# Optimization experiments

Measured on AMD Instinct MI355X. Metric: run time of the kernel, lower is better.

## Reference

```python
import jax, jax.numpy as jnp
import numpy as np

T, H, E, F, K, FS = 2048, 2048, 64, 512, 8, 512


def setup_inputs() -> dict:
    key = jax.random.key(0)
    ks = jax.random.split(key, 6)
    s = 0.02
    return {
        "hidden_states": jax.random.normal(ks[0], (T, H), jnp.float32),
        # merged gate: E router logits + 1 shared-expert gate logit
        "W_gate": jax.random.normal(ks[1], (H, E + 1), jnp.float32) * s,
        # per-expert merged gate_up proj: [E, H, 2F]
        "W_gate_up": jax.random.normal(ks[2], (E, H, 2 * F), jnp.float32) * s,
        "W_down": jax.random.normal(ks[3], (E, F, H), jnp.float32) * s,
        # shared expert
        "Ws_gate_up": jax.random.normal(ks[4], (H, 2 * FS), jnp.float32) * s,
        "Ws_down": jax.random.normal(ks[5], (FS, H), jnp.float32) * s,
    }


def reference(hidden_states, W_gate, W_gate_up, W_down, Ws_gate_up, Ws_down):
    x = hidden_states  # [T, H]
    logits_all = x @ W_gate                      # [T, E+1]
    router_logits = logits_all[:, :E]
    shared_gate_logit = logits_all[:, E:]        # [T, 1]

    # FusedMoE routing: softmax -> top_k -> renormalize (norm_topk_prob=True)
    probs = jax.nn.softmax(router_logits.astype(jnp.float32), axis=-1)
    topk_w, topk_idx = jax.lax.top_k(probs, K)   # [T, K]
    topk_w = topk_w / jnp.sum(topk_w, axis=-1, keepdims=True)
    # dense combine weights [T, E] (zero for unselected experts)
    combine = jnp.zeros((T, E), probs.dtype).at[
        jnp.arange(T)[:, None], topk_idx].set(topk_w)

    # grouped expert GEMMs (dense reference: every expert sees all tokens,
    # combine-weights zero-out unrouted pairs)
    gu = jnp.einsum('th,ehf->etf', x, W_gate_up)   # [E, T, 2F]
    g, u = jnp.split(gu, 2, axis=-1)
    act = jax.nn.silu(g) * u                       # [E, T, F]
    # apply combine weight before down-proj to avoid [E, T, H] intermediate
    act = act * combine.T[:, :, None].astype(act.dtype)
    routed = jnp.einsum('etf,efh->th', act, W_down)  # [T, H]

    # shared expert (Qwen3NextMLP with sigmoid expert_gate)
    sgu = x @ Ws_gate_up                           # [T, 2FS]
    sg, su = jnp.split(sgu, 2, axis=-1)
    shared = (jax.nn.silu(sg) * su) @ Ws_down      # [T, H]
    shared = jax.nn.sigmoid(shared_gate_logit) * shared

    return shared + routed.astype(x.dtype)
```

## Files before the change

kernel.cpp:

```cpp
#include <hip/hip_runtime.h>
#include <hip/hip_bf16.h>
#include <math.h>

#define T_TOK 2048
#define H_DIM 2048
#define E_NUM 64
#define F_DIM 512
#define K_TOP 8
#define FS_DIM 512
#define NROWS (T_TOK * K_TOP)

typedef __attribute__((ext_vector_type(8))) short short8v;
typedef __attribute__((ext_vector_type(4))) float f32x4;

static __device__ __forceinline__ unsigned short f2bf(float f) {
    unsigned int u = __float_as_uint(f);
    u += 0x7fff + ((u >> 16) & 1);
    return (unsigned short)(u >> 16);
}

#define BCHUNK(row, k8) ((((k8) ^ ((row) + ((row) >> 3)))) & 7)
#define ASW32(r) (((r) >> 1) & 3)

typedef const unsigned int __attribute__((address_space(1))) gu32;
typedef unsigned int __attribute__((address_space(3))) lu32;
#define GLDS16(gsrc, ldst) \
    __builtin_amdgcn_global_load_lds((gu32*)(gsrc), (lu32*)(ldst), 16, 0, 0)

__global__ __launch_bounds__(256) void cvt_bf16_kernel(
    const float* __restrict__ in, unsigned short* __restrict__ out, int n8)
{
    int i = blockIdx.x * 256 + threadIdx.x;
    if (i < n8) {
        const float4* p = (const float4*)(in + (size_t)i * 8);
        float4 v0 = p[0], v1 = p[1];
        ushort4 a = make_ushort4(f2bf(v0.x), f2bf(v0.y), f2bf(v0.z), f2bf(v0.w));
        ushort4 b = make_ushort4(f2bf(v1.x), f2bf(v1.y), f2bf(v1.z), f2bf(v1.w));
        ushort4* q = (ushort4*)(out + (size_t)i * 8);
        q[0] = a; q[1] = b;
    }
}

__global__ __launch_bounds__(64) void router_kernel(
    const float* __restrict__ x, const float* __restrict__ Wg,
    int* __restrict__ topk_idx, float* __restrict__ topk_w,
    float* __restrict__ sgate, int* __restrict__ counts)
{
    const int t = blockIdx.x;
    const int lane = threadIdx.x;
    const float* xr = x + (size_t)t * H_DIM;

    float a0 = 0.f, a1 = 0.f, a2 = 0.f, a3 = 0.f;
    for (int h = 0; h < H_DIM; h += 4) {
        float4 xv = *(const float4*)&xr[h];
        a0 += xv.x * Wg[(h + 0) * 65 + lane];
        a1 += xv.y * Wg[(h + 1) * 65 + lane];
        a2 += xv.z * Wg[(h + 2) * 65 + lane];
        a3 += xv.w * Wg[(h + 3) * 65 + lane];
    }
    float logit = (a0 + a1) + (a2 + a3);

    float a64 = 0.f;
    for (int h = lane; h < H_DIM; h += 64) a64 += xr[h] * Wg[h * 65 + 64];
#pragma unroll
    for (int off = 32; off >= 1; off >>= 1) a64 += __shfl_xor(a64, off);

    float v = logit;
    float selv[K_TOP]; int seli[K_TOP];
#pragma unroll
    for (int k = 0; k < K_TOP; ++k) {
        float mv = v; int mi = lane;
#pragma unroll
        for (int off = 32; off >= 1; off >>= 1) {
            float ov = __shfl_xor(mv, off);
            int   oi = __shfl_xor(mi, off);
            if (ov > mv || (ov == mv && oi < mi)) { mv = ov; mi = oi; }
        }
        selv[k] = mv; seli[k] = mi;
        if (lane == mi) v = -INFINITY;
    }

    if (lane == 0) {
        float m = selv[0];
        float w[K_TOP]; float s = 0.f;
#pragma unroll
        for (int k = 0; k < K_TOP; ++k) { w[k] = __expf(selv[k] - m); s += w[k]; }
        float inv = 1.f / s;
#pragma unroll
        for (int k = 0; k < K_TOP; ++k) {
            topk_idx[t * K_TOP + k] = seli[k];
            topk_w[t * K_TOP + k] = w[k] * inv;
            atomicAdd(&counts[seli[k]], 1);
        }
        sgate[t] = 1.f / (1.f + __expf(-a64));
    }
}

__global__ __launch_bounds__(256) void bucket_kernel(
    const int* __restrict__ topk_idx, const float* __restrict__ topk_w,
    const int* __restrict__ counts, int* __restrict__ offsets,
    int* __restrict__ bucket_tok, float* __restrict__ bucket_w)
{
    const int e = blockIdx.x, thr = threadIdx.x;
    __shared__ int cnt[256];
    __shared__ int base_s;
    const int q0 = thr * 64;
    int c = 0;
    for (int q = 0; q < 64; ++q) c += (topk_idx[q0 + q] == e) ? 1 : 0;
    cnt[thr] = c;
    __syncthreads();
    if (thr == 0) {
        int off = 0;
        for (int i = 0; i < e; ++i) off += counts[i];
        offsets[e] = off;
        base_s = off;
        int run = 0;
        for (int i = 0; i < 256; ++i) { int tval = cnt[i]; cnt[i] = run; run += tval; }
    }
    __syncthreads();
    int pos = base_s + cnt[thr];
    for (int q = 0; q < 64; ++q) {
        int pp = q0 + q;
        if (topk_idx[pp] == e) {
            bucket_tok[pos] = pp >> 3;
            bucket_w[pos] = topk_w[pp];
            ++pos;
        }
    }
}

template<bool ROUTED>
__global__ __launch_bounds__(512, 4) void gu_mfma_kernel(
    const unsigned short* __restrict__ xb,
    const float* __restrict__ Wall,
    const int* __restrict__ counts, const int* __restrict__ offsets,
    const int* __restrict__ bucket_tok, const float* __restrict__ bucket_w,
    unsigned short* __restrict__ actout)
{
    constexpr int BM = 256;
    __shared__ __align__(16) unsigned short As[2][BM * 32];
    __shared__ __align__(16) unsigned short Bs[2][128 * 64];
    __shared__ int   toksS[BM];
    __shared__ float twsS[BM];

    const int tid  = threadIdx.x;
    const int lane = tid & 63;
    const int wid  = tid >> 6;
    const int wm = wid >> 1, wn = wid & 1;
    const int lrow = lane & 15, lhi = lane >> 4;

    int cblk, mt, ne, base;
    const float* W;
    if (ROUTED) {
        int nw = (blockIdx.x & 7) * ((int)gridDim.x >> 3) + (blockIdx.x >> 3);
        int e = nw >> 4; mt = (nw >> 3) & 1; cblk = nw & 7;
        ne = counts[e]; base = offsets[e];
        if (mt * BM >= ne) return;
        W = Wall + (size_t)e * H_DIM * (2 * F_DIM);
    } else {
        cblk = blockIdx.x; mt = blockIdx.y;
        ne = T_TOK; base = 0;
        W = Wall;
    }
    const int c0 = cblk * 64;

    const int n4 = (tid & 31) * 4;
    const int kq = (tid >> 5) * 4;
    const int grp = n4 >> 5;
    const int srccol = c0 + (grp >> 1) * 32 + (n4 & 31) + ((grp & 1) ? F_DIM : 0);
    int wrB[4];
#pragma unroll
    for (int cc = 0; cc < 4; ++cc) {
        int n = n4 + cc;
        wrB[cc] = n * 64 + BCHUNK(n, kq >> 3) * 8 + (kq & 7);
    }
    int rdB[4][2];
#pragma unroll
    for (int fn = 0; fn < 4; ++fn) {
        int r = wn * 64 + fn * 16 + lrow;
#pragma unroll
        for (int ks = 0; ks < 2; ++ks) {
            int kc = ks * 4 + lhi;
            rdB[fn][ks] = r * 64 + BCHUNK(r, kc) * 8;
        }
    }
    int rdA[4];
#pragma unroll
    for (int fm = 0; fm < 4; ++fm) {
        int arow = wm * 64 + fm * 16 + lrow;
        rdA[fm] = arow * 32 + ((lhi ^ ASW32(arow)) << 3);
    }
    const int ar0 = wid * 32 + (lane >> 2);
    const int ar1 = ar0 + 16;
    const int NT   = H_DIM / 64;
    const int SMAX = H_DIM / 32;
    const int m0_stride = ROUTED ? (2 * BM) : ((int)gridDim.y * BM);

    for (int m0 = mt * BM; m0 < ne; m0 += m0_stride) {
        __syncthreads();
        if (tid < BM) {
            int idx = m0 + tid; bool v = idx < ne;
            if (ROUTED) {
                toksS[tid] = v ? bucket_tok[base + idx] : bucket_tok[base];
                twsS[tid]  = v ? bucket_w[base + idx] : 0.f;
            } else {
                toksS[tid] = v ? idx : (T_TOK - 1);
                twsS[tid]  = 1.f;
            }
        }
        __syncthreads();

        const int src0 = toksS[ar0] * H_DIM + (((lane & 3) ^ ASW32(ar0)) << 3);
        const int src1 = toksS[ar1] * H_DIM + (((lane & 3) ^ ASW32(ar1)) << 3);

        f32x4 acc[4][4];
#pragma unroll
        for (int i = 0; i < 4; ++i)
#pragma unroll
            for (int j = 0; j < 4; ++j) acc[i][j] = (f32x4){0.f, 0.f, 0.f, 0.f};

        float4 bq[4];
#pragma unroll
        for (int i = 0; i < 4; ++i)
            bq[i] = *(const float4*)&W[(size_t)(kq + i) * (2 * F_DIM) + srccol];
        GLDS16(xb + src0, &As[0][(wid * 32) * 32]);
        GLDS16(xb + src1, &As[0][(wid * 32 + 16) * 32]);
#pragma unroll
        for (int cc = 0; cc < 4; ++cc)
            *(ushort4*)&Bs[0][wrB[cc]] = make_ushort4(
                f2bf(((const float*)&bq[0])[cc]), f2bf(((const float*)&bq[1])[cc]),
                f2bf(((const float*)&bq[2])[cc]), f2bf(((const float*)&bq[3])[cc]));
#pragma unroll
        for (int i = 0; i < 4; ++i)
            bq[i] = *(const float4*)&W[(size_t)(64 + kq + i) * (2 * F_DIM) + srccol];
        __syncthreads();

        for (int s = 0; s < SMAX; ++s) {
            const int kt = s >> 1;
            if (s + 1 < SMAX) {
                const int kof = (s + 1) * 32;
                GLDS16(xb + src0 + kof, &As[(s + 1) & 1][(wid * 32) * 32]);
                GLDS16(xb + src1 + kof, &As[(s + 1) & 1][(wid * 32 + 16) * 32]);
            }
            if ((s & 1) && (kt + 1 < NT)) {
#pragma unroll
                for (int cc = 0; cc < 4; ++cc)
                    *(ushort4*)&Bs[(kt + 1) & 1][wrB[cc]] = make_ushort4(
                        f2bf(((const float*)&bq[0])[cc]), f2bf(((const float*)&bq[1])[cc]),
                        f2bf(((const float*)&bq[2])[cc]), f2bf(((const float*)&bq[3])[cc]));
                int knx = (kt + 2 < NT) ? (kt + 2) * 64 : (NT - 1) * 64;
#pragma unroll
                for (int i = 0; i < 4; ++i)
                    bq[i] = *(const float4*)&W[(size_t)(knx + kq + i) * (2 * F_DIM) + srccol];
            }
            __builtin_amdgcn_sched_barrier(0);
            const unsigned short* A_ = As[s & 1];
            const unsigned short* B_ = Bs[kt & 1];
            const int ks = s & 1;
            short8v bf[4];
#pragma unroll
            for (int fn = 0; fn < 4; ++fn) bf[fn] = *(const short8v*)&B_[rdB[fn][ks]];
#pragma unroll
            for (int fm = 0; fm < 4; ++fm) {
                short8v af = *(const short8v*)&A_[rdA[fm]];
#pragma unroll
                for (int fn = 0; fn < 4; ++fn)
                    acc[fm][fn] = __builtin_amdgcn_mfma_f32_16x16x32_bf16(af, bf[fn], acc[fm][fn], 0, 0, 0);
            }
            __syncthreads();
        }

#pragma unroll
        for (int fm = 0; fm < 4; ++fm) {
#pragma unroll
            for (int p = 0; p < 2; ++p) {
                const int acol = c0 + wn * 32 + p * 16 + lrow;
#pragma unroll
                for (int i = 0; i < 4; ++i) {
                    int ml = wm * 64 + fm * 16 + lhi * 4 + i;
                    int idx = m0 + ml;
                    if (idx < ne) {
                        float gv = acc[fm][p][i], uv = acc[fm][p + 2][i];
                        float sg = gv / (1.f + __expf(-gv));
                        float val = sg * uv * twsS[ml];
                        size_t orow = ROUTED ? (size_t)(base + idx) : (size_t)idx;
                        actout[orow * F_DIM + acol] = f2bf(val);
                    }
                }
            }
        }
    }
}

template<bool ROUTED>
__global__ __launch_bounds__(512, 4) void down_mfma_kernel(
    const unsigned short* __restrict__ actb,
    const float* __restrict__ Wall,
    const int* __restrict__ counts, const int* __restrict__ offsets,
    const int* __restrict__ bucket_tok, const float* __restrict__ sgate,
    float* __restrict__ out)
{
    constexpr int BM = 256;
    __shared__ __align__(16) unsigned short As[2][BM * 32];
    __shared__ __align__(16) unsigned short Bs[2][128 * 64];
    __shared__ int   toksS[BM];
    __shared__ float sgS[BM];

    const int tid  = threadIdx.x;
    const int lane = tid & 63;
    const int wid  = tid >> 6;
    const int wm = wid >> 1, wn = wid & 1;
    const int lrow = lane & 15, lhi = lane >> 4;

    int cblk, mt, ne, base;
    const float* W;
    if (ROUTED) {
        int nw = (blockIdx.x & 7) * ((int)gridDim.x >> 3) + (blockIdx.x >> 3);
        int e = nw >> 5; mt = (nw >> 4) & 1; cblk = nw & 15;
        ne = counts[e]; base = offsets[e];
        if (mt * BM >= ne) return;
        W = Wall + (size_t)e * F_DIM * H_DIM;
    } else {
        cblk = blockIdx.x; mt = blockIdx.y;
        ne = T_TOK; base = 0;
        W = Wall;
    }
    const int c0 = cblk * 128;

    const int n4 = (tid & 31) * 4;
    const int kq = (tid >> 5) * 4;
    const int srccol = c0 + n4;
    int wrB[4];
#pragma unroll
    for (int cc = 0; cc < 4; ++cc) {
        int n = n4 + cc;
        wrB[cc] = n * 64 + BCHUNK(n, kq >> 3) * 8 + (kq & 7);
    }
    int rdB[4][2];
#pragma unroll
    for (int fn = 0; fn < 4; ++fn) {
        int r = wn * 64 + fn * 16 + lrow;
#pragma unroll
        for (int ks = 0; ks < 2; ++ks) {
            int kc = ks * 4 + lhi;
            rdB[fn][ks] = r * 64 + BCHUNK(r, kc) * 8;
        }
    }
    int rdA[4];
#pragma unroll
    for (int fm = 0; fm < 4; ++fm) {
        int arow = wm * 64 + fm * 16 + lrow;
        rdA[fm] = arow * 32 + ((lhi ^ ASW32(arow)) << 3);
    }
    const int ar0 = wid * 32 + (lane >> 2);
    const int ar1 = ar0 + 16;
    const int NT   = F_DIM / 64;
    const int SMAX = F_DIM / 32;
    const int m0_stride = ROUTED ? (2 * BM) : ((int)gridDim.y * BM);

    for (int m0 = mt * BM; m0 < ne; m0 += m0_stride) {
        __syncthreads();
        if (tid < BM) {
            int idx = m0 + tid;
            if (ROUTED) {
                toksS[tid] = (idx < ne) ? bucket_tok[base + idx] : 0;
            } else {
                sgS[tid] = sgate[(idx < ne) ? idx : (T_TOK - 1)];
            }
        }
        __syncthreads();

        int g0 = ROUTED ? min(base + m0 + ar0, NROWS - 1) : min(m0 + ar0, T_TOK - 1);
        int g1 = ROUTED ? min(base + m0 + ar1, NROWS - 1) : min(m0 + ar1, T_TOK - 1);
        const int src0 = g0 * F_DIM + (((lane & 3) ^ ASW32(ar0)) << 3);
        const int src1 = g1 * F_DIM + (((lane & 3) ^ ASW32(ar1)) << 3);

        f32x4 acc[4][4];
#pragma unroll
        for (int i = 0; i < 4; ++i)
#pragma unroll
            for (int j = 0; j < 4; ++j) acc[i][j] = (f32x4){0.f, 0.f, 0.f, 0.f};

        float4 bq[4];
#pragma unroll
        for (int i = 0; i < 4; ++i)
            bq[i] = *(const float4*)&W[(size_t)(kq + i) * H_DIM + srccol];
        GLDS16(actb + src0, &As[0][(wid * 32) * 32]);
        GLDS16(actb + src1, &As[0][(wid * 32 + 16) * 32]);
#pragma unroll
        for (int cc = 0; cc < 4; ++cc)
            *(ushort4*)&Bs[0][wrB[cc]] = make_ushort4(
                f2bf(((const float*)&bq[0])[cc]), f2bf(((const float*)&bq[1])[cc]),
                f2bf(((const float*)&bq[2])[cc]), f2bf(((const float*)&bq[3])[cc]));
#pragma unroll
        for (int i = 0; i < 4; ++i)
            bq[i] = *(const float4*)&W[(size_t)(64 + kq + i) * H_DIM + srccol];
        __syncthreads();

        for (int s = 0; s < SMAX; ++s) {
            const int kt = s >> 1;
            if (s + 1 < SMAX) {
                const int kof = (s + 1) * 32;
                GLDS16(actb + src0 + kof, &As[(s + 1) & 1][(wid * 32) * 32]);
                GLDS16(actb + src1 + kof, &As[(s + 1) & 1][(wid * 32 + 16) * 32]);
            }
            if ((s & 1) && (kt + 1 < NT)) {
#pragma unroll
                for (int cc = 0; cc < 4; ++cc)
                    *(ushort4*)&Bs[(kt + 1) & 1][wrB[cc]] = make_ushort4(
                        f2bf(((const float*)&bq[0])[cc]), f2bf(((const float*)&bq[1])[cc]),
                        f2bf(((const float*)&bq[2])[cc]), f2bf(((const float*)&bq[3])[cc]));
                int knx = (kt + 2 < NT) ? (kt + 2) * 64 : (NT - 1) * 64;
#pragma unroll
                for (int i = 0; i < 4; ++i)
                    bq[i] = *(const float4*)&W[(size_t)(knx + kq + i) * H_DIM + srccol];
            }
            __builtin_amdgcn_sched_barrier(0);
            const unsigned short* A_ = As[s & 1];
            const unsigned short* B_ = Bs[kt & 1];
            const int ks = s & 1;
            short8v bf[4];
#pragma unroll
            for (int fn = 0; fn < 4; ++fn) bf[fn] = *(const short8v*)&B_[rdB[fn][ks]];
#pragma unroll
            for (int fm = 0; fm < 4; ++fm) {
                short8v af = *(const short8v*)&A_[rdA[fm]];
#pragma unroll
                for (int fn = 0; fn < 4; ++fn)
                    acc[fm][fn] = __builtin_amdgcn_mfma_f32_16x16x32_bf16(af, bf[fn], acc[fm][fn], 0, 0, 0);
            }
            __syncthreads();
        }

#pragma unroll
        for (int fm = 0; fm < 4; ++fm) {
#pragma unroll
            for (int fn = 0; fn < 4; ++fn) {
                int col = c0 + wn * 64 + fn * 16 + lrow;
#pragma unroll
                for (int i = 0; i < 4; ++i) {
                    int ml = wm * 64 + fm * 16 + lhi * 4 + i;
                    int idx = m0 + ml;
                    if (idx < ne) {
                        if (ROUTED) {
                            atomicAdd(&out[(size_t)toksS[ml] * H_DIM + col], acc[fm][fn][i]);
                        } else {
                            out[(size_t)idx * H_DIM + col] = sgS[ml] * acc[fm][fn][i];
                        }
                    }
                }
            }
        }
    }
}

extern "C" void kernel_launch(void* const* d_in, const int* in_sizes, int n_in,
                              void* d_out, int out_size, void* d_ws, size_t ws_size,
                              hipStream_t stream) {
    const float* x    = (const float*)d_in[0];
    const float* Wg   = (const float*)d_in[1];
    const float* Wgu  = (const float*)d_in[2];
    const float* Wd   = (const float*)d_in[3];
    const float* Wsgu = (const float*)d_in[4];
    const float* Wsd  = (const float*)d_in[5];
    float* out = (float*)d_out;

    char* p = (char*)d_ws;
    auto alloc = [&](size_t bytes) {
        char* r = p;
        p += (bytes + 255) & ~(size_t)255;
        return r;
    };
    int*   topk_idx   = (int*)  alloc((size_t)T_TOK * K_TOP * sizeof(int));
    float* topk_w     = (float*)alloc((size_t)T_TOK * K_TOP * sizeof(float));
    float* sgate      = (float*)alloc((size_t)T_TOK * sizeof(float));
    int*   counts     = (int*)  alloc((size_t)E_NUM * sizeof(int));
    int*   offsets    = (int*)  alloc((size_t)E_NUM * sizeof(int));
    int*   bucket_tok = (int*)  alloc((size_t)NROWS * sizeof(int));
    float* bucket_w   = (float*)alloc((size_t)NROWS * sizeof(float));
    unsigned short* xb    = (unsigned short*)alloc((size_t)T_TOK * H_DIM * sizeof(short));
    unsigned short* act_r = (unsigned short*)alloc((size_t)NROWS * F_DIM * sizeof(short));
    unsigned short* act_s = (unsigned short*)alloc((size_t)T_TOK * FS_DIM * sizeof(short));

    hipMemsetAsync(counts, 0, E_NUM * sizeof(int), stream);
    cvt_bf16_kernel<<<(T_TOK * H_DIM / 8 + 255) / 256, 256, 0, stream>>>(x, xb, T_TOK * H_DIM / 8);
    router_kernel<<<T_TOK, 64, 0, stream>>>(x, Wg, topk_idx, topk_w, sgate, counts);
    bucket_kernel<<<E_NUM, 256, 0, stream>>>(topk_idx, topk_w, counts, offsets, bucket_tok, bucket_w);

    gu_mfma_kernel<true><<<8 * E_NUM * 2, 512, 0, stream>>>(
        xb, Wgu, counts, offsets, bucket_tok, bucket_w, act_r);
    gu_mfma_kernel<false><<<dim3(8, T_TOK / 256), 512, 0, stream>>>(
        xb, Wsgu, counts, offsets, bucket_tok, bucket_w, act_s);

    down_mfma_kernel<false><<<dim3(16, T_TOK / 256), 512, 0, stream>>>(
        act_s, Wsd, counts, offsets, bucket_tok, sgate, out);
    down_mfma_kernel<true><<<16 * E_NUM * 2, 512, 0, stream>>>(
        act_r, Wd, counts, offsets, bucket_tok, sgate, out);
}
```

Measured before the change: 741.4 us.

## Pre-transpose weights to bf16 and use LDS-free direct-load MFMA GEMMs

```diff
diff --git a/kernel.cpp b/kernel.cpp
--- a/kernel.cpp
+++ b/kernel.cpp
@@ -21,7 +21,6 @@
 
 #define BCHUNK(row, k8) ((((k8) ^ ((row) + ((row) >> 3)))) & 7)
 #define ASW32(r) (((r) >> 1) & 3)
-
 typedef const unsigned int __attribute__((address_space(1))) gu32;
 typedef unsigned int __attribute__((address_space(3))) lu32;
 #define GLDS16(gsrc, ldst) \
@@ -129,10 +128,216 @@
     }
 }
 
+__global__ __launch_bounds__(256) void transpose_cvt_kernel(
+    const float* __restrict__ in, unsigned short* __restrict__ out,
+    int R, int C)
+{
+    const int e = blockIdx.z;
+    in  += (size_t)e * R * C;
+    out += (size_t)e * R * C;
+    const int c0 = blockIdx.x * 64, r0 = blockIdx.y * 64;
+    __shared__ unsigned short tile[64][72];
+    const int t = threadIdx.x;
+    const int cc = (t & 15) * 4;
+#pragma unroll
+    for (int i = 0; i < 4; ++i) {
+        int r = (t >> 4) + i * 16;
+        float4 v = *(const float4*)&in[(size_t)(r0 + r) * C + c0 + cc];
+        tile[cc + 0][r] = f2bf(v.x);
+        tile[cc + 1][r] = f2bf(v.y);
+        tile[cc + 2][r] = f2bf(v.z);
+        tile[cc + 3][r] = f2bf(v.w);
+    }
+    __syncthreads();
+    const int c = t >> 2, j = t & 3;
+    uint4 v0 = *(const uint4*)&tile[c][j * 16];
+    uint4 v1 = *(const uint4*)&tile[c][j * 16 + 8];
+    uint4* dst = (uint4*)&out[(size_t)(c0 + c) * R + r0 + j * 16];
+    dst[0] = v0; dst[1] = v1;
+}
+
+__global__ __launch_bounds__(512, 4) void gu_direct_kernel(
+    const unsigned short* __restrict__ xb,
+    const unsigned short* __restrict__ WT,
+    const int* __restrict__ counts, const int* __restrict__ offsets,
+    const int* __restrict__ bucket_tok, const float* __restrict__ bucket_w,
+    unsigned short* __restrict__ act_r, unsigned short* __restrict__ act_s)
+{
+    const int tid = threadIdx.x, lane = tid & 63, wid = tid >> 6;
+    const int wm = wid >> 1, wn = wid & 1;
+    const int lrow = lane & 15, lhi = lane >> 4;
+    const int eu = blockIdx.x >> 3;
+    const int ct = blockIdx.x & 7;
+    const int c0 = ct * 64;
+    const bool sh = (eu >= E_NUM);
+    const int e = sh ? E_NUM : eu;
+    int ne, base, m0beg, m0end;
+    if (sh) { ne = T_TOK; base = 0; m0beg = (eu - E_NUM) * 256; m0end = m0beg + 256; }
+    else    { ne = counts[eu]; base = offsets[eu]; m0beg = 0; m0end = ne; }
+    const unsigned short* We = WT + (size_t)e * (2 * F_DIM) * H_DIM;
+
+    __shared__ int   toksS[256];
+    __shared__ float twsS[256];
+
+    const unsigned short* bp[4];
+    bp[0] = We + (size_t)(c0 + wn * 32 + lrow) * H_DIM;
+    bp[1] = We + (size_t)(c0 + wn * 32 + 16 + lrow) * H_DIM;
+    bp[2] = We + (size_t)(F_DIM + c0 + wn * 32 + lrow) * H_DIM;
+    bp[3] = We + (size_t)(F_DIM + c0 + wn * 32 + 16 + lrow) * H_DIM;
+
+    for (int m0 = m0beg; m0 < m0end; m0 += 256) {
+        __syncthreads();
+        if (tid < 256) {
+            int idx = m0 + tid; bool v = idx < ne;
+            if (sh) { toksS[tid] = v ? idx : 0; twsS[tid] = 1.f; }
+            else {
+                toksS[tid] = v ? bucket_tok[base + idx] : bucket_tok[base];
+                twsS[tid]  = v ? bucket_w[base + idx] : 0.f;
+            }
+        }
+        __syncthreads();
+
+        const unsigned short* ap[4];
+#pragma unroll
+        for (int fm = 0; fm < 4; ++fm)
+            ap[fm] = xb + (size_t)toksS[wm * 64 + fm * 16 + lrow] * H_DIM;
+
+        f32x4 acc[4][4];
+#pragma unroll
+        for (int i = 0; i < 4; ++i)
+#pragma unroll
+            for (int j = 0; j < 4; ++j) acc[i][j] = (f32x4){0.f, 0.f, 0.f, 0.f};
+
+#pragma unroll 2
+        for (int k0 = 0; k0 < H_DIM; k0 += 32) {
+            const int ko = k0 + lhi * 8;
+            short8v a[4], b[4];
+#pragma unroll
+            for (int i = 0; i < 4; ++i) a[i] = *(const short8v*)(ap[i] + ko);
+#pragma unroll
+            for (int i = 0; i < 4; ++i) b[i] = *(const short8v*)(bp[i] + ko);
+#pragma unroll
+            for (int fm = 0; fm < 4; ++fm)
+#pragma unroll
+                for (int fn = 0; fn < 4; ++fn)
+                    acc[fm][fn] = __builtin_amdgcn_mfma_f32_16x16x32_bf16(
+                        a[fm], b[fn], acc[fm][fn], 0, 0, 0);
+        }
+
+#pragma unroll
+        for (int fm = 0; fm < 4; ++fm) {
+#pragma unroll
+            for (int p = 0; p < 2; ++p) {
+                const int acol = c0 + wn * 32 + p * 16 + lrow;
+#pragma unroll
+                for (int i = 0; i < 4; ++i) {
+                    int ml = wm * 64 + fm * 16 + lhi * 4 + i;
+                    int idx = m0 + ml;
+                    if (idx < ne) {
+                        float gv = acc[fm][p][i], uv = acc[fm][p + 2][i];
+                        float sg = gv / (1.f + __expf(-gv));
+                        float val = sg * uv * twsS[ml];
+                        if (sh) act_s[(size_t)idx * F_DIM + acol] = f2bf(val);
+                        else    act_r[(size_t)(base + idx) * F_DIM + acol] = f2bf(val);
+                    }
+                }
+            }
+        }
+    }
+}
+
+__global__ __launch_bounds__(512, 4) void down_direct_kernel(
+    const unsigned short* __restrict__ act_r,
+    const unsigned short* __restrict__ act_s,
+    const unsigned short* __restrict__ WT,
+    const int* __restrict__ counts, const int* __restrict__ offsets,
+    const int* __restrict__ bucket_tok, const float* __restrict__ sgate,
+    float* __restrict__ out)
+{
+    const int tid = threadIdx.x, lane = tid & 63, wid = tid >> 6;
+    const int wm = wid >> 1, wn = wid & 1;
+    const int lrow = lane & 15, lhi = lane >> 4;
+    const int eu = blockIdx.x >> 4;
+    const int ct = blockIdx.x & 15;
+    const int c0 = ct * 128;
+    const bool sh = (eu >= E_NUM);
+    const int e = sh ? E_NUM : eu;
+    int ne, base, m0beg, m0end;
+    if (sh) { ne = T_TOK; base = 0; m0beg = (eu - E_NUM) * 256; m0end = m0beg + 256; }
+    else    { ne = counts[eu]; base = offsets[eu]; m0beg = 0; m0end = ne; }
+    const unsigned short* We = WT + (size_t)e * H_DIM * F_DIM;
+
+    __shared__ int   toksS[256];
+    __shared__ float sgS[256];
+
+    const unsigned short* bp[4];
+#pragma unroll
+    for (int fn = 0; fn < 4; ++fn)
+        bp[fn] = We + (size_t)(c0 + wn * 64 + fn * 16 + lrow) * F_DIM;
+
+    for (int m0 = m0beg; m0 < m0end; m0 += 256) {
+        __syncthreads();
+        if (tid < 256) {
+            int idx = m0 + tid;
+            if (sh) sgS[tid] = sgate[(idx < ne) ? idx : 0];
+            else    toksS[tid] = (idx < ne) ? bucket_tok[base + idx] : 0;
+        }
+        __syncthreads();
+
+        const unsigned short* ap[4];
+#pragma unroll
+        for (int fm = 0; fm < 4; ++fm) {
+            int r = wm * 64 + fm * 16 + lrow;
+            if (sh) ap[fm] = act_s + (size_t)min(m0 + r, T_TOK - 1) * F_DIM;
+            else    ap[fm] = act_r + (size_t)min(base + m0 + r, NROWS - 1) * F_DIM;
+        }
+
+        f32x4 acc[4][4];
+#pragma unroll
+        for (int i = 0; i < 4; ++i)
+#pragma unroll
+            for (int j = 0; j < 4; ++j) acc[i][j] = (f32x4){0.f, 0.f, 0.f, 0.f};
+
+#pragma unroll 2
+        for (int k0 = 0; k0 < F_DIM; k0 += 32) {
+            const int ko = k0 + lhi * 8;
+            short8v a[4], b[4];
+#pragma unroll
+            for (int i = 0; i < 4; ++i) a[i] = *(const short8v*)(ap[i] + ko);
+#pragma unroll
+            for (int i = 0; i < 4; ++i) b[i] = *(const short8v*)(bp[i] + ko);
+#pragma unroll
+            for (int fm = 0; fm < 4; ++fm)
+#pragma unroll
+                for (int fn = 0; fn < 4; ++fn)
+                    acc[fm][fn] = __builtin_amdgcn_mfma_f32_16x16x32_bf16(
+                        a[fm], b[fn], acc[fm][fn], 0, 0, 0);
+        }
+
+#pragma unroll
+        for (int fm = 0; fm < 4; ++fm) {
+#pragma unroll
+            for (int fn = 0; fn < 4; ++fn) {
+                int col = c0 + wn * 64 + fn * 16 + lrow;
+#pragma unroll
+                for (int i = 0; i < 4; ++i) {
+                    int ml = wm * 64 + fm * 16 + lhi * 4 + i;
+                    int idx = m0 + ml;
+                    if (idx < ne) {
+                        if (sh)
+                            atomicAdd(&out[(size_t)idx * H_DIM + col], sgS[ml] * acc[fm][fn][i]);
+                        else
+                            atomicAdd(&out[(size_t)toksS[ml] * H_DIM + col], acc[fm][fn][i]);
+                    }
+                }
+            }
+        }
+    }
+}
+
 template<bool ROUTED>
-__global__ __launch_bounds__(512, 4) void gu_mfma_kernel(
-    const unsigned short* __restrict__ xb,
-    const float* __restrict__ Wall,
+__global__ __launch_bounds__(512, 4) void fb_gu_kernel(
+    const unsigned short* __restrict__ xb, const float* __restrict__ Wall,
     const int* __restrict__ counts, const int* __restrict__ offsets,
     const int* __restrict__ bucket_tok, const float* __restrict__ bucket_w,
     unsigned short* __restrict__ actout)
@@ -140,15 +345,11 @@
     constexpr int BM = 256;
     __shared__ __align__(16) unsigned short As[2][BM * 32];
     __shared__ __align__(16) unsigned short Bs[2][128 * 64];
-    __shared__ int   toksS[BM];
+    __shared__ int toksS[BM];
     __shared__ float twsS[BM];
-
-    const int tid  = threadIdx.x;
-    const int lane = tid & 63;
-    const int wid  = tid >> 6;
+    const int tid = threadIdx.x, lane = tid & 63, wid = tid >> 6;
     const int wm = wid >> 1, wn = wid & 1;
     const int lrow = lane & 15, lhi = lane >> 4;
-
     int cblk, mt, ne, base;
     const float* W;
     if (ROUTED) {
@@ -158,14 +359,10 @@
         if (mt * BM >= ne) return;
         W = Wall + (size_t)e * H_DIM * (2 * F_DIM);
     } else {
-        cblk = blockIdx.x; mt = blockIdx.y;
-        ne = T_TOK; base = 0;
-        W = Wall;
+        cblk = blockIdx.x; mt = blockIdx.y; ne = T_TOK; base = 0; W = Wall;
     }
     const int c0 = cblk * 64;
-
-    const int n4 = (tid & 31) * 4;
-    const int kq = (tid >> 5) * 4;
+    const int n4 = (tid & 31) * 4, kq = (tid >> 5) * 4;
     const int grp = n4 >> 5;
     const int srccol = c0 + (grp >> 1) * 32 + (n4 & 31) + ((grp & 1) ? F_DIM : 0);
     int wrB[4];
@@ -190,35 +387,25 @@
         int arow = wm * 64 + fm * 16 + lrow;
         rdA[fm] = arow * 32 + ((lhi ^ ASW32(arow)) << 3);
     }
-    const int ar0 = wid * 32 + (lane >> 2);
-    const int ar1 = ar0 + 16;
-    const int NT   = H_DIM / 64;
-    const int SMAX = H_DIM / 32;
-    const int m0_stride = ROUTED ? (2 * BM) : ((int)gridDim.y * BM);
-
-    for (int m0 = mt * BM; m0 < ne; m0 += m0_stride) {
+    const int ar0 = wid * 32 + (lane >> 2), ar1 = ar0 + 16;
+    const int NT = H_DIM / 64, SMAX = H_DIM / 32;
+    for (int m0 = mt * BM; m0 < ne; m0 += (ROUTED ? 2 * BM : (int)gridDim.y * BM)) {
         __syncthreads();
         if (tid < BM) {
             int idx = m0 + tid; bool v = idx < ne;
             if (ROUTED) {
                 toksS[tid] = v ? bucket_tok[base + idx] : bucket_tok[base];
-                twsS[tid]  = v ? bucket_w[base + idx] : 0.f;
-            } else {
-                toksS[tid] = v ? idx : (T_TOK - 1);
-                twsS[tid]  = 1.f;
-            }
-        }
-        __syncthreads();
-
+                twsS[tid] = v ? bucket_w[base + idx] : 0.f;
+            } else { toksS[tid] = v ? idx : (T_TOK - 1); twsS[tid] = 1.f; }
+        }
+        __syncthreads();
         const int src0 = toksS[ar0] * H_DIM + (((lane & 3) ^ ASW32(ar0)) << 3);
         const int src1 = toksS[ar1] * H_DIM + (((lane & 3) ^ ASW32(ar1)) << 3);
-
         f32x4 acc[4][4];
 #pragma unroll
         for (int i = 0; i < 4; ++i)
 #pragma unroll
             for (int j = 0; j < 4; ++j) acc[i][j] = (f32x4){0.f, 0.f, 0.f, 0.f};
-
         float4 bq[4];
 #pragma unroll
         for (int i = 0; i < 4; ++i)
@@ -234,7 +421,6 @@
         for (int i = 0; i < 4; ++i)
             bq[i] = *(const float4*)&W[(size_t)(64 + kq + i) * (2 * F_DIM) + srccol];
         __syncthreads();
-
         for (int s = 0; s < SMAX; ++s) {
             const int kt = s >> 1;
             if (s + 1 < SMAX) {
@@ -269,7 +455,6 @@
             }
             __syncthreads();
         }
-
 #pragma unroll
         for (int fm = 0; fm < 4; ++fm) {
 #pragma unroll
@@ -293,9 +478,8 @@
 }
 
 template<bool ROUTED>
-__global__ __launch_bounds__(512, 4) void down_mfma_kernel(
-    const unsigned short* __restrict__ actb,
-    const float* __restrict__ Wall,
+__global__ __launch_bounds__(512, 4) void fb_down_kernel(
+    const unsigned short* __restrict__ actb, const float* __restrict__ Wall,
     const int* __restrict__ counts, const int* __restrict__ offsets,
     const int* __restrict__ bucket_tok, const float* __restrict__ sgate,
     float* __restrict__ out)
@@ -303,15 +487,11 @@
     constexpr int BM = 256;
     __shared__ __align__(16) unsigned short As[2][BM * 32];
     __shared__ __align__(16) unsigned short Bs[2][128 * 64];
-    __shared__ int   toksS[BM];
+    __shared__ int toksS[BM];
     __shared__ float sgS[BM];
-
-    const int tid  = threadIdx.x;
-    const int lane = tid & 63;
-    const int wid  = tid >> 6;
+    const int tid = threadIdx.x, lane = tid & 63, wid = tid >> 6;
     const int wm = wid >> 1, wn = wid & 1;
     const int lrow = lane & 15, lhi = lane >> 4;
-
     int cblk, mt, ne, base;
     const float* W;
     if (ROUTED) {
@@ -321,14 +501,10 @@
         if (mt * BM >= ne) return;
         W = Wall + (size_t)e * F_DIM * H_DIM;
     } else {
-        cblk = blockIdx.x; mt = blockIdx.y;
-        ne = T_TOK; base = 0;
-        W = Wall;
+        cblk = blockIdx.x; mt = blockIdx.y; ne = T_TOK; base = 0; W = Wall;
     }
     const int c0 = cblk * 128;
-
-    const int n4 = (tid & 31) * 4;
-    const int kq = (tid >> 5) * 4;
+    const int n4 = (tid & 31) * 4, kq = (tid >> 5) * 4;
     const int srccol = c0 + n4;
     int wrB[4];
 #pragma unroll
@@ -352,35 +528,25 @@
         int arow = wm * 64 + fm * 16 + lrow;
         rdA[fm] = arow * 32 + ((lhi ^ ASW32(arow)) << 3);
     }
-    const int ar0 = wid * 32 + (lane >> 2);
-    const int ar1 = ar0 + 16;
-    const int NT   = F_DIM / 64;
-    const int SMAX = F_DIM / 32;
-    const int m0_stride = ROUTED ? (2 * BM) : ((int)gridDim.y * BM);
-
-    for (int m0 = mt * BM; m0 < ne; m0 += m0_stride) {
+    const int ar0 = wid * 32 + (lane >> 2), ar1 = ar0 + 16;
+    const int NT = F_DIM / 64, SMAX = F_DIM / 32;
+    for (int m0 = mt * BM; m0 < ne; m0 += (ROUTED ? 2 * BM : (int)gridDim.y * BM)) {
         __syncthreads();
         if (tid < BM) {
             int idx = m0 + tid;
-            if (ROUTED) {
-                toksS[tid] = (idx < ne) ? bucket_tok[base + idx] : 0;
-            } else {
-                sgS[tid] = sgate[(idx < ne) ? idx : (T_TOK - 1)];
-            }
-        }
-        __syncthreads();
-
+            if (ROUTED) toksS[tid] = (idx < ne) ? bucket_tok[base + idx] : 0;
+            else sgS[tid] = sgate[(idx < ne) ? idx : (T_TOK - 1)];
+        }
+        __syncthreads();
         int g0 = ROUTED ? min(base + m0 + ar0, NROWS - 1) : min(m0 + ar0, T_TOK - 1);
         int g1 = ROUTED ? min(base + m0 + ar1, NROWS - 1) : min(m0 + ar1, T_TOK - 1);
         const int src0 = g0 * F_DIM + (((lane & 3) ^ ASW32(ar0)) << 3);
         const int src1 = g1 * F_DIM + (((lane & 3) ^ ASW32(ar1)) << 3);
-
         f32x4 acc[4][4];
 #pragma unroll
         for (int i = 0; i < 4; ++i)
 #pragma unroll
             for (int j = 0; j < 4; ++j) acc[i][j] = (f32x4){0.f, 0.f, 0.f, 0.f};
-
         float4 bq[4];
 #pragma unroll
         for (int i = 0; i < 4; ++i)
@@ -396,7 +562,6 @@
         for (int i = 0; i < 4; ++i)
             bq[i] = *(const float4*)&W[(size_t)(64 + kq + i) * H_DIM + srccol];
         __syncthreads();
-
         for (int s = 0; s < SMAX; ++s) {
             const int kt = s >> 1;
             if (s + 1 < SMAX) {
@@ -431,7 +596,6 @@
             }
             __syncthreads();
         }
-
 #pragma unroll
         for (int fm = 0; fm < 4; ++fm) {
 #pragma unroll
@@ -442,11 +606,8 @@
                     int ml = wm * 64 + fm * 16 + lhi * 4 + i;
                     int idx = m0 + ml;
                     if (idx < ne) {
-                        if (ROUTED) {
-                            atomicAdd(&out[(size_t)toksS[ml] * H_DIM + col], acc[fm][fn][i]);
-                        } else {
-                            out[(size_t)idx * H_DIM + col] = sgS[ml] * acc[fm][fn][i];
-                        }
+                        if (ROUTED) atomicAdd(&out[(size_t)toksS[ml] * H_DIM + col], acc[fm][fn][i]);
+                        else out[(size_t)idx * H_DIM + col] = sgS[ml] * acc[fm][fn][i];
                     }
                 }
             }
@@ -465,11 +626,11 @@
     const float* Wsd  = (const float*)d_in[5];
     float* out = (float*)d_out;
 
-    char* p = (char*)d_ws;
+    size_t used = 0;
     auto alloc = [&](size_t bytes) {
-        char* r = p;
-        p += (bytes + 255) & ~(size_t)255;
-        return r;
+        size_t off = used;
+        used += (bytes + 255) & ~(size_t)255;
+        return (char*)d_ws + off;
     };
     int*   topk_idx   = (int*)  alloc((size_t)T_TOK * K_TOP * sizeof(int));
     float* topk_w     = (float*)alloc((size_t)T_TOK * K_TOP * sizeof(float));
@@ -478,22 +639,41 @@
     int*   offsets    = (int*)  alloc((size_t)E_NUM * sizeof(int));
     int*   bucket_tok = (int*)  alloc((size_t)NROWS * sizeof(int));
     float* bucket_w   = (float*)alloc((size_t)NROWS * sizeof(float));
-    unsigned short* xb    = (unsigned short*)alloc((size_t)T_TOK * H_DIM * sizeof(short));
-    unsigned short* act_r = (unsigned short*)alloc((size_t)NROWS * F_DIM * sizeof(short));
-    unsigned short* act_s = (unsigned short*)alloc((size_t)T_TOK * FS_DIM * sizeof(short));
+    unsigned short* xb    = (unsigned short*)alloc((size_t)T_TOK * H_DIM * 2);
+    unsigned short* act_r = (unsigned short*)alloc((size_t)NROWS * F_DIM * 2);
+    unsigned short* act_s = (unsigned short*)alloc((size_t)T_TOK * FS_DIM * 2);
+    unsigned short* WTgu = (unsigned short*)alloc((size_t)65 * (2 * F_DIM) * H_DIM * 2);
+    unsigned short* WTd  = (unsigned short*)alloc((size_t)65 * H_DIM * F_DIM * 2);
+    const bool big = (used <= ws_size);
 
     hipMemsetAsync(counts, 0, E_NUM * sizeof(int), stream);
     cvt_bf16_kernel<<<(T_TOK * H_DIM / 8 + 255) / 256, 256, 0, stream>>>(x, xb, T_TOK * H_DIM / 8);
     router_kernel<<<T_TOK, 64, 0, stream>>>(x, Wg, topk_idx, topk_w, sgate, counts);
     bucket_kernel<<<E_NUM, 256, 0, stream>>>(topk_idx, topk_w, counts, offsets, bucket_tok, bucket_w);
 
-    gu_mfma_kernel<true><<<8 * E_NUM * 2, 512, 0, stream>>>(
-        xb, Wgu, counts, offsets, bucket_tok, bucket_w, act_r);
-    gu_mfma_kernel<false><<<dim3(8, T_TOK / 256), 512, 0, stream>>>(
-        xb, Wsgu, counts, offsets, bucket_tok, bucket_w, act_s);
-
-    down_mfma_kernel<false><<<dim3(16, T_TOK / 256), 512, 0, stream>>>(
-        act_s, Wsd, counts, offsets, bucket_tok, sgate, out);
-    down_mfma_kernel<true><<<16 * E_NUM * 2, 512, 0, stream>>>(
-        act_r, Wd, counts, offsets, bucket_tok, sgate, out);
-}
+    if (big) {
+        hipMemsetAsync(out, 0, (size_t)T_TOK * H_DIM * sizeof(float), stream);
+        transpose_cvt_kernel<<<dim3((2 * F_DIM) / 64, H_DIM / 64, E_NUM), 256, 0, stream>>>(
+            Wgu, WTgu, H_DIM, 2 * F_DIM);
+        transpose_cvt_kernel<<<dim3((2 * FS_DIM) / 64, H_DIM / 64, 1), 256, 0, stream>>>(
+            Wsgu, WTgu + (size_t)64 * (2 * F_DIM) * H_DIM, H_DIM, 2 * FS_DIM);
+        transpose_cvt_kernel<<<dim3(H_DIM / 64, F_DIM / 64, E_NUM), 256, 0, stream>>>(
+            Wd, WTd, F_DIM, H_DIM);
+        transpose_cvt_kernel<<<dim3(H_DIM / 64, FS_DIM / 64, 1), 256, 0, stream>>>(
+            Wsd, WTd + (size_t)64 * H_DIM * F_DIM, FS_DIM, H_DIM);
+
+        gu_direct_kernel<<<72 * 8, 512, 0, stream>>>(
+            xb, WTgu, counts, offsets, bucket_tok, bucket_w, act_r, act_s);
+        down_direct_kernel<<<72 * 16, 512, 0, stream>>>(
+            act_r, act_s, WTd, counts, offsets, bucket_tok, sgate, out);
+    } else {
+        fb_gu_kernel<true><<<8 * E_NUM * 2, 512, 0, stream>>>(
+            xb, Wgu, counts, offsets, bucket_tok, bucket_w, act_r);
+        fb_gu_kernel<false><<<dim3(8, T_TOK / 256), 512, 0, stream>>>(
+            xb, Wsgu, counts, offsets, bucket_tok, bucket_w, act_s);
+        fb_down_kernel<false><<<dim3(16, T_TOK / 256), 512, 0, stream>>>(
+            act_s, Wsd, counts, offsets, bucket_tok, sgate, out);
+        fb_down_kernel<true><<<16 * E_NUM * 2, 512, 0, stream>>>(
+            act_r, Wd, counts, offsets, bucket_tok, sgate, out);
+    }
+}
```

Result: slower. 1.152 ms (+55.4%).

## Restructure expert GEMMs to 128-row tiles with 64-wide K steps and 256 threads

Applied to the files above, without the earlier changes.

```diff
diff --git a/kernel.cpp b/kernel.cpp
--- a/kernel.cpp
+++ b/kernel.cpp
@@ -20,7 +20,7 @@
 }
 
 #define BCHUNK(row, k8) ((((k8) ^ ((row) + ((row) >> 3)))) & 7)
-#define ASW32(r) (((r) >> 1) & 3)
+#define ASWZ(row) (((row) + ((row) >> 3)) & 7)
 
 typedef const unsigned int __attribute__((address_space(1))) gu32;
 typedef unsigned int __attribute__((address_space(3))) lu32;
@@ -130,15 +130,15 @@
 }
 
 template<bool ROUTED>
-__global__ __launch_bounds__(512, 4) void gu_mfma_kernel(
+__global__ __launch_bounds__(256, 2) void gu_mfma_kernel(
     const unsigned short* __restrict__ xb,
     const float* __restrict__ Wall,
     const int* __restrict__ counts, const int* __restrict__ offsets,
     const int* __restrict__ bucket_tok, const float* __restrict__ bucket_w,
     unsigned short* __restrict__ actout)
 {
-    constexpr int BM = 256;
-    __shared__ __align__(16) unsigned short As[2][BM * 32];
+    constexpr int BM = 128;
+    __shared__ __align__(16) unsigned short As[2][BM * 64];
     __shared__ __align__(16) unsigned short Bs[2][128 * 64];
     __shared__ int   toksS[BM];
     __shared__ float twsS[BM];
@@ -149,30 +149,29 @@
     const int wm = wid >> 1, wn = wid & 1;
     const int lrow = lane & 15, lhi = lane >> 4;
 
-    int cblk, mt, ne, base;
+    int cblk, ne, base;
     const float* W;
     if (ROUTED) {
         int nw = (blockIdx.x & 7) * ((int)gridDim.x >> 3) + (blockIdx.x >> 3);
-        int e = nw >> 4; mt = (nw >> 3) & 1; cblk = nw & 7;
+        int e = nw >> 3; cblk = nw & 7;
         ne = counts[e]; base = offsets[e];
-        if (mt * BM >= ne) return;
         W = Wall + (size_t)e * H_DIM * (2 * F_DIM);
     } else {
-        cblk = blockIdx.x; mt = blockIdx.y;
+        cblk = blockIdx.x;
         ne = T_TOK; base = 0;
         W = Wall;
     }
     const int c0 = cblk * 64;
 
     const int n4 = (tid & 31) * 4;
-    const int kq = (tid >> 5) * 4;
+    const int kq = (tid >> 5) * 8;
     const int grp = n4 >> 5;
     const int srccol = c0 + (grp >> 1) * 32 + (n4 & 31) + ((grp & 1) ? F_DIM : 0);
     int wrB[4];
 #pragma unroll
     for (int cc = 0; cc < 4; ++cc) {
         int n = n4 + cc;
-        wrB[cc] = n * 64 + BCHUNK(n, kq >> 3) * 8 + (kq & 7);
+        wrB[cc] = n * 64 + BCHUNK(n, kq >> 3) * 8;
     }
     int rdB[4][2];
 #pragma unroll
@@ -184,19 +183,22 @@
             rdB[fn][ks] = r * 64 + BCHUNK(r, kc) * 8;
         }
     }
-    int rdA[4];
+    int rdA[4][2];
 #pragma unroll
     for (int fm = 0; fm < 4; ++fm) {
         int arow = wm * 64 + fm * 16 + lrow;
-        rdA[fm] = arow * 32 + ((lhi ^ ASW32(arow)) << 3);
-    }
-    const int ar0 = wid * 32 + (lane >> 2);
-    const int ar1 = ar0 + 16;
-    const int NT   = H_DIM / 64;
-    const int SMAX = H_DIM / 32;
-    const int m0_stride = ROUTED ? (2 * BM) : ((int)gridDim.y * BM);
-
-    for (int m0 = mt * BM; m0 < ne; m0 += m0_stride) {
+#pragma unroll
+        for (int ks = 0; ks < 2; ++ks) {
+            int kc = ks * 4 + lhi;
+            rdA[fm][ks] = arow * 64 + ((kc ^ ASWZ(arow)) & 7) * 8;
+        }
+    }
+    const int NT = H_DIM / 64;
+
+    const int m0_beg = ROUTED ? 0 : blockIdx.y * BM;
+    const int m0_end = ROUTED ? ne : m0_beg + BM;
+
+    for (int m0 = m0_beg; m0 < m0_end; m0 += BM) {
         __syncthreads();
         if (tid < BM) {
             int idx = m0 + tid; bool v = idx < ne;
@@ -210,8 +212,12 @@
         }
         __syncthreads();
 
-        const int src0 = toksS[ar0] * H_DIM + (((lane & 3) ^ ASW32(ar0)) << 3);
-        const int src1 = toksS[ar1] * H_DIM + (((lane & 3) ^ ASW32(ar1)) << 3);
+        int asrc[4];
+#pragma unroll
+        for (int i = 0; i < 4; ++i) {
+            int row = wid * 32 + i * 8 + (lane >> 3);
+            asrc[i] = toksS[row] * H_DIM + (((lane & 7) ^ ASWZ(row)) << 3);
+        }
 
         f32x4 acc[4][4];
 #pragma unroll
@@ -219,53 +225,62 @@
 #pragma unroll
             for (int j = 0; j < 4; ++j) acc[i][j] = (f32x4){0.f, 0.f, 0.f, 0.f};
 
-        float4 bq[4];
+        float4 bq[8];
+#pragma unroll
+        for (int j = 0; j < 8; ++j)
+            bq[j] = *(const float4*)&W[(size_t)(kq + j) * (2 * F_DIM) + srccol];
+#pragma unroll
+        for (int cc = 0; cc < 4; ++cc) {
+            short8v pk;
+#pragma unroll
+            for (int j = 0; j < 8; ++j)
+                pk[j] = (short)f2bf(((const float*)&bq[j])[cc]);
+            *(short8v*)&Bs[0][wrB[cc]] = pk;
+        }
+#pragma unroll
+        for (int j = 0; j < 8; ++j)
+            bq[j] = *(const float4*)&W[(size_t)(64 + kq + j) * (2 * F_DIM) + srccol];
 #pragma unroll
         for (int i = 0; i < 4; ++i)
-            bq[i] = *(const float4*)&W[(size_t)(kq + i) * (2 * F_DIM) + srccol];
-        GLDS16(xb + src0, &As[0][(wid * 32) * 32]);
-        GLDS16(xb + src1, &As[0][(wid * 32 + 16) * 32]);
-#pragma unroll
-        for (int cc = 0; cc < 4; ++cc)
-            *(ushort4*)&Bs[0][wrB[cc]] = make_ushort4(
-                f2bf(((const float*)&bq[0])[cc]), f2bf(((const float*)&bq[1])[cc]),
-                f2bf(((const float*)&bq[2])[cc]), f2bf(((const float*)&bq[3])[cc]));
-#pragma unroll
-        for (int i = 0; i < 4; ++i)
-            bq[i] = *(const float4*)&W[(size_t)(64 + kq + i) * (2 * F_DIM) + srccol];
+            GLDS16(xb + asrc[i], &As[0][(wid * 32 + i * 8) * 64]);
         __syncthreads();
 
-        for (int s = 0; s < SMAX; ++s) {
-            const int kt = s >> 1;
-            if (s + 1 < SMAX) {
-                const int kof = (s + 1) * 32;
-                GLDS16(xb + src0 + kof, &As[(s + 1) & 1][(wid * 32) * 32]);
-                GLDS16(xb + src1 + kof, &As[(s + 1) & 1][(wid * 32 + 16) * 32]);
-            }
-            if ((s & 1) && (kt + 1 < NT)) {
-#pragma unroll
-                for (int cc = 0; cc < 4; ++cc)
-                    *(ushort4*)&Bs[(kt + 1) & 1][wrB[cc]] = make_ushort4(
-                        f2bf(((const float*)&bq[0])[cc]), f2bf(((const float*)&bq[1])[cc]),
-                        f2bf(((const float*)&bq[2])[cc]), f2bf(((const float*)&bq[3])[cc]));
-                int knx = (kt + 2 < NT) ? (kt + 2) * 64 : (NT - 1) * 64;
+        for (int kt = 0; kt < NT; ++kt) {
+            const int k0 = kt * 64;
+            if (kt + 1 < NT) {
 #pragma unroll
                 for (int i = 0; i < 4; ++i)
-                    bq[i] = *(const float4*)&W[(size_t)(knx + kq + i) * (2 * F_DIM) + srccol];
+                    GLDS16(xb + asrc[i] + k0 + 64, &As[(kt + 1) & 1][(wid * 32 + i * 8) * 64]);
+                unsigned short* nB = Bs[(kt + 1) & 1];
+#pragma unroll
+                for (int cc = 0; cc < 4; ++cc) {
+                    short8v pk;
+#pragma unroll
+                    for (int j = 0; j < 8; ++j)
+                        pk[j] = (short)f2bf(((const float*)&bq[j])[cc]);
+                    *(short8v*)&nB[wrB[cc]] = pk;
+                }
+                int knx = (kt + 2 < NT) ? (k0 + 128) : (k0 + 64);
+#pragma unroll
+                for (int j = 0; j < 8; ++j)
+                    bq[j] = *(const float4*)&W[(size_t)(knx + kq + j) * (2 * F_DIM) + srccol];
             }
             __builtin_amdgcn_sched_barrier(0);
-            const unsigned short* A_ = As[s & 1];
+            const unsigned short* A_ = As[kt & 1];
             const unsigned short* B_ = Bs[kt & 1];
-            const int ks = s & 1;
-            short8v bf[4];
-#pragma unroll
-            for (int fn = 0; fn < 4; ++fn) bf[fn] = *(const short8v*)&B_[rdB[fn][ks]];
-#pragma unroll
-            for (int fm = 0; fm < 4; ++fm) {
-                short8v af = *(const short8v*)&A_[rdA[fm]];
-#pragma unroll
-                for (int fn = 0; fn < 4; ++fn)
-                    acc[fm][fn] = __builtin_amdgcn_mfma_f32_16x16x32_bf16(af, bf[fn], acc[fm][fn], 0, 0, 0);
+#pragma unroll
+            for (int ks = 0; ks < 2; ++ks) {
+                short8v bf[4];
+#pragma unroll
+                for (int fn = 0; fn < 4; ++fn) bf[fn] = *(const short8v*)&B_[rdB[fn][ks]];
+#pragma unroll
+                for (int fm = 0; fm < 4; ++fm) {
+                    short8v af = *(const short8v*)&A_[rdA[fm][ks]];
+#pragma unroll
+                    for (int fn = 0; fn < 4; ++fn)
+                        acc[fm][fn] = __builtin_amdgcn_mfma_f32_16x16x32_bf16(
+                            af, bf[fn], acc[fm][fn], 0, 0, 0);
+                }
             }
             __syncthreads();
         }
@@ -293,15 +308,15 @@
 }
 
 template<bool ROUTED>
-__global__ __launch_bounds__(512, 4) void down_mfma_kernel(
+__global__ __launch_bounds__(256, 2) void down_mfma_kernel(
     const unsigned short* __restrict__ actb,
     const float* __restrict__ Wall,
     const int* __restrict__ counts, const int* __restrict__ offsets,
     const int* __restrict__ bucket_tok, const float* __restrict__ sgate,
     float* __restrict__ out)
 {
-    constexpr int BM = 256;
-    __shared__ __align__(16) unsigned short As[2][BM * 32];
+    constexpr int BM = 128;
+    __shared__ __align__(16) unsigned short As[2][BM * 64];
     __shared__ __align__(16) unsigned short Bs[2][128 * 64];
     __shared__ int   toksS[BM];
     __shared__ float sgS[BM];
@@ -312,29 +327,28 @@
     const int wm = wid >> 1, wn = wid & 1;
     const int lrow = lane & 15, lhi = lane >> 4;
 
-    int cblk, mt, ne, base;
+    int cblk, ne, base;
     const float* W;
     if (ROUTED) {
         int nw = (blockIdx.x & 7) * ((int)gridDim.x >> 3) + (blockIdx.x >> 3);
-        int e = nw >> 5; mt = (nw >> 4) & 1; cblk = nw & 15;
+        int e = nw >> 4; cblk = nw & 15;
         ne = counts[e]; base = offsets[e];
-        if (mt * BM >= ne) return;
         W = Wall + (size_t)e * F_DIM * H_DIM;
     } else {
-        cblk = blockIdx.x; mt = blockIdx.y;
+        cblk = blockIdx.x;
         ne = T_TOK; base = 0;
         W = Wall;
     }
     const int c0 = cblk * 128;
 
     const int n4 = (tid & 31) * 4;
-    const int kq = (tid >> 5) * 4;
+    const int kq = (tid >> 5) * 8;
     const int srccol = c0 + n4;
     int wrB[4];
 #pragma unroll
     for (int cc = 0; cc < 4; ++cc) {
         int n = n4 + cc;
-        wrB[cc] = n * 64 + BCHUNK(n, kq >> 3) * 8 + (kq & 7);
+        wrB[cc] = n * 64 + BCHUNK(n, kq >> 3) * 8;
     }
     int rdB[4][2];
 #pragma unroll
@@ -346,19 +360,22 @@
             rdB[fn][ks] = r * 64 + BCHUNK(r, kc) * 8;
         }
     }
-    int rdA[4];
+    int rdA[4][2];
 #pragma unroll
     for (int fm = 0; fm < 4; ++fm) {
         int arow = wm * 64 + fm * 16 + lrow;
-        rdA[fm] = arow * 32 + ((lhi ^ ASW32(arow)) << 3);
-    }
-    const int ar0 = wid * 32 + (lane >> 2);
-    const int ar1 = ar0 + 16;
-    const int NT   = F_DIM / 64;
-    const int SMAX = F_DIM / 32;
-    const int m0_stride = ROUTED ? (2 * BM) : ((int)gridDim.y * BM);
-
-    for (int m0 = mt * BM; m0 < ne; m0 += m0_stride) {
+#pragma unroll
+        for (int ks = 0; ks < 2; ++ks) {
+            int kc = ks * 4 + lhi;
+            rdA[fm][ks] = arow * 64 + ((kc ^ ASWZ(arow)) & 7) * 8;
+        }
+    }
+    const int NT = F_DIM / 64;
+
+    const int m0_beg = ROUTED ? 0 : blockIdx.y * BM;
+    const int m0_end = ROUTED ? ne : m0_beg + BM;
+
+    for (int m0 = m0_beg; m0 < m0_end; m0 += BM) {
         __syncthreads();
         if (tid < BM) {
             int idx = m0 + tid;
@@ -370,10 +387,14 @@
         }
         __syncthreads();
 
-        int g0 = ROUTED ? min(base + m0 + ar0, NROWS - 1) : min(m0 + ar0, T_TOK - 1);
-        int g1 = ROUTED ? min(base + m0 + ar1, NROWS - 1) : min(m0 + ar1, T_TOK - 1);
-        const int src0 = g0 * F_DIM + (((lane & 3) ^ ASW32(ar0)) << 3);
-        const int src1 = g1 * F_DIM + (((lane & 3) ^ ASW32(ar1)) << 3);
+        int asrc[4];
+#pragma unroll
+        for (int i = 0; i < 4; ++i) {
+            int row = wid * 32 + i * 8 + (lane >> 3);
+            int grow = ROUTED ? min(base + m0 + row, NROWS - 1)
+                              : min(m0 + row, T_TOK - 1);
+            asrc[i] = grow * F_DIM + (((lane & 7) ^ ASWZ(row)) << 3);
+        }
 
         f32x4 acc[4][4];
 #pragma unroll
@@ -381,53 +402,62 @@
 #pragma unroll
             for (int j = 0; j < 4; ++j) acc[i][j] = (f32x4){0.f, 0.f, 0.f, 0.f};
 
-        float4 bq[4];
+        float4 bq[8];
+#pragma unroll
+        for (int j = 0; j < 8; ++j)
+            bq[j] = *(const float4*)&W[(size_t)(kq + j) * H_DIM + srccol];
+#pragma unroll
+        for (int cc = 0; cc < 4; ++cc) {
+            short8v pk;
+#pragma unroll
+            for (int j = 0; j < 8; ++j)
+                pk[j] = (short)f2bf(((const float*)&bq[j])[cc]);
+            *(short8v*)&Bs[0][wrB[cc]] = pk;
+        }
+#pragma unroll
+        for (int j = 0; j < 8; ++j)
+            bq[j] = *(const float4*)&W[(size_t)(64 + kq + j) * H_DIM + srccol];
 #pragma unroll
         for (int i = 0; i < 4; ++i)
-            bq[i] = *(const float4*)&W[(size_t)(kq + i) * H_DIM + srccol];
-        GLDS16(actb + src0, &As[0][(wid * 32) * 32]);
-        GLDS16(actb + src1, &As[0][(wid * 32 + 16) * 32]);
-#pragma unroll
-        for (int cc = 0; cc < 4; ++cc)
-            *(ushort4*)&Bs[0][wrB[cc]] = make_ushort4(
-                f2bf(((const float*)&bq[0])[cc]), f2bf(((const float*)&bq[1])[cc]),
-                f2bf(((const float*)&bq[2])[cc]), f2bf(((const float*)&bq[3])[cc]));
-#pragma unroll
-        for (int i = 0; i < 4; ++i)
-            bq[i] = *(const float4*)&W[(size_t)(64 + kq + i) * H_DIM + srccol];
+            GLDS16(actb + asrc[i], &As[0][(wid * 32 + i * 8) * 64]);
         __syncthreads();
 
-        for (int s = 0; s < SMAX; ++s) {
-            const int kt = s >> 1;
-            if (s + 1 < SMAX) {
-                const int kof = (s + 1) * 32;
-                GLDS16(actb + src0 + kof, &As[(s + 1) & 1][(wid * 32) * 32]);
-                GLDS16(actb + src1 + kof, &As[(s + 1) & 1][(wid * 32 + 16) * 32]);
-            }
-            if ((s & 1) && (kt + 1 < NT)) {
-#pragma unroll
-                for (int cc = 0; cc < 4; ++cc)
-                    *(ushort4*)&Bs[(kt + 1) & 1][wrB[cc]] = make_ushort4(
-                        f2bf(((const float*)&bq[0])[cc]), f2bf(((const float*)&bq[1])[cc]),
-                        f2bf(((const float*)&bq[2])[cc]), f2bf(((const float*)&bq[3])[cc]));
-                int knx = (kt + 2 < NT) ? (kt + 2) * 64 : (NT - 1) * 64;
+        for (int kt = 0; kt < NT; ++kt) {
+            const int k0 = kt * 64;
+            if (kt + 1 < NT) {
 #pragma unroll
                 for (int i = 0; i < 4; ++i)
-                    bq[i] = *(const float4*)&W[(size_t)(knx + kq + i) * H_DIM + srccol];
+                    GLDS16(actb + asrc[i] + k0 + 64, &As[(kt + 1) & 1][(wid * 32 + i * 8) * 64]);
+                unsigned short* nB = Bs[(kt + 1) & 1];
+#pragma unroll
+                for (int cc = 0; cc < 4; ++cc) {
+                    short8v pk;
+#pragma unroll
+                    for (int j = 0; j < 8; ++j)
+                        pk[j] = (short)f2bf(((const float*)&bq[j])[cc]);
+                    *(short8v*)&nB[wrB[cc]] = pk;
+                }
+                int knx = (kt + 2 < NT) ? (k0 + 128) : (k0 + 64);
+#pragma unroll
+                for (int j = 0; j < 8; ++j)
+                    bq[j] = *(const float4*)&W[(size_t)(knx + kq + j) * H_DIM + srccol];
             }
             __builtin_amdgcn_sched_barrier(0);
-            const unsigned short* A_ = As[s & 1];
+            const unsigned short* A_ = As[kt & 1];
             const unsigned short* B_ = Bs[kt & 1];
-            const int ks = s & 1;
-            short8v bf[4];
-#pragma unroll
-            for (int fn = 0; fn < 4; ++fn) bf[fn] = *(const short8v*)&B_[rdB[fn][ks]];
-#pragma unroll
-            for (int fm = 0; fm < 4; ++fm) {
-                short8v af = *(const short8v*)&A_[rdA[fm]];
-#pragma unroll
-                for (int fn = 0; fn < 4; ++fn)
-                    acc[fm][fn] = __builtin_amdgcn_mfma_f32_16x16x32_bf16(af, bf[fn], acc[fm][fn], 0, 0, 0);
+#pragma unroll
+            for (int ks = 0; ks < 2; ++ks) {
+                short8v bf[4];
+#pragma unroll
+                for (int fn = 0; fn < 4; ++fn) bf[fn] = *(const short8v*)&B_[rdB[fn][ks]];
+#pragma unroll
+                for (int fm = 0; fm < 4; ++fm) {
+                    short8v af = *(const short8v*)&A_[rdA[fm][ks]];
+#pragma unroll
+                    for (int fn = 0; fn < 4; ++fn)
+                        acc[fm][fn] = __builtin_amdgcn_mfma_f32_16x16x32_bf16(
+                            af, bf[fn], acc[fm][fn], 0, 0, 0);
+                }
             }
             __syncthreads();
         }
@@ -442,11 +472,10 @@
                     int ml = wm * 64 + fm * 16 + lhi * 4 + i;
                     int idx = m0 + ml;
                     if (idx < ne) {
-                        if (ROUTED) {
+                        if (ROUTED)
                             atomicAdd(&out[(size_t)toksS[ml] * H_DIM + col], acc[fm][fn][i]);
-                        } else {
+                        else
                             out[(size_t)idx * H_DIM + col] = sgS[ml] * acc[fm][fn][i];
-                        }
                     }
                 }
             }
@@ -478,22 +507,22 @@
     int*   offsets    = (int*)  alloc((size_t)E_NUM * sizeof(int));
     int*   bucket_tok = (int*)  alloc((size_t)NROWS * sizeof(int));
     float* bucket_w   = (float*)alloc((size_t)NROWS * sizeof(float));
-    unsigned short* xb    = (unsigned short*)alloc((size_t)T_TOK * H_DIM * sizeof(short));
-    unsigned short* act_r = (unsigned short*)alloc((size_t)NROWS * F_DIM * sizeof(short));
-    unsigned short* act_s = (unsigned short*)alloc((size_t)T_TOK * FS_DIM * sizeof(short));
+    unsigned short* xb    = (unsigned short*)alloc((size_t)T_TOK * H_DIM * 2);
+    unsigned short* act_r = (unsigned short*)alloc((size_t)NROWS * F_DIM * 2);
+    unsigned short* act_s = (unsigned short*)alloc((size_t)T_TOK * FS_DIM * 2);
 
     hipMemsetAsync(counts, 0, E_NUM * sizeof(int), stream);
     cvt_bf16_kernel<<<(T_TOK * H_DIM / 8 + 255) / 256, 256, 0, stream>>>(x, xb, T_TOK * H_DIM / 8);
     router_kernel<<<T_TOK, 64, 0, stream>>>(x, Wg, topk_idx, topk_w, sgate, counts);
     bucket_kernel<<<E_NUM, 256, 0, stream>>>(topk_idx, topk_w, counts, offsets, bucket_tok, bucket_w);
 
-    gu_mfma_kernel<true><<<8 * E_NUM * 2, 512, 0, stream>>>(
+    gu_mfma_kernel<true><<<8 * E_NUM, 256, 0, stream>>>(
         xb, Wgu, counts, offsets, bucket_tok, bucket_w, act_r);
-    gu_mfma_kernel<false><<<dim3(8, T_TOK / 256), 512, 0, stream>>>(
+    gu_mfma_kernel<false><<<dim3(8, T_TOK / 128), 256, 0, stream>>>(
         xb, Wsgu, counts, offsets, bucket_tok, bucket_w, act_s);
 
-    down_mfma_kernel<false><<<dim3(16, T_TOK / 256), 512, 0, stream>>>(
+    down_mfma_kernel<false><<<dim3(16, T_TOK / 128), 256, 0, stream>>>(
         act_s, Wsd, counts, offsets, bucket_tok, sgate, out);
-    down_mfma_kernel<true><<<16 * E_NUM * 2, 512, 0, stream>>>(
+    down_mfma_kernel<true><<<16 * E_NUM, 256, 0, stream>>>(
         act_r, Wd, counts, offsets, bucket_tok, sgate, out);
 }
```

Measured after the change: 705.7 us (median of 2 runs). -4.8%, faster.
